# Kernel tuning notes

Hardware: AMD Instinct MI355X
Metric: run time of the kernel (lower is better)

Reference implementation:

```python
import jax, jax.numpy as jnp
import numpy as np

D_MODEL = 512
D_INNER = 1024           # expand=2 * d_model
HEADDIM = 1024           # headdim = 2*hidden_dim -> nheads = 1
NHEADS = 1
D_STATE = 128            # Mamba2 default
D_CONV = 4               # Mamba2 default
CONV_DIM = D_INNER + 2 * D_STATE   # 1280
D_IN_PROJ = 2 * D_INNER + 2 * D_STATE + NHEADS  # 2305
BATCH, SEQ = 8, 2048
EPS = 1e-5


def setup_inputs() -> dict:
    key = jax.random.key(0)
    ks = jax.random.split(key, 8)
    x = jax.random.normal(ks[0], (BATCH, SEQ, D_MODEL), dtype=jnp.float32)
    rnn_state = jnp.zeros((1, BATCH, D_MODEL), dtype=jnp.float32)
    W_in = jax.random.normal(ks[1], (D_MODEL, D_IN_PROJ), dtype=jnp.float32) * 0.02
    conv_w = jax.random.normal(ks[2], (CONV_DIM, D_CONV), dtype=jnp.float32) * 0.2
    conv_b = jnp.zeros((CONV_DIM,), dtype=jnp.float32)
    dt_bias = jax.random.normal(ks[3], (NHEADS,), dtype=jnp.float32) * 0.1
    # A in (-16, -1): A_log = log(uniform(1,16))
    A_log = jnp.log(jax.random.uniform(ks[4], (NHEADS,), minval=1.0, maxval=16.0, dtype=jnp.float32))
    D = jnp.ones((NHEADS,), dtype=jnp.float32)
    norm_w = jnp.ones((D_INNER,), dtype=jnp.float32)
    W_out = jax.random.normal(ks[5], (D_INNER, D_MODEL), dtype=jnp.float32) * 0.02
    return {"x": x, "rnn_state": rnn_state, "W_in": W_in, "conv_w": conv_w,
            "conv_b": conv_b, "dt_bias": dt_bias, "A_log": A_log, "D": D,
            "norm_w": norm_w, "W_out": W_out}


def _mamba2_forward(x, W_in, conv_w, conv_b, dt_bias, A_log, D, norm_w, W_out):
    Bsz, T, _ = x.shape
    zxbcdt = x @ W_in                              # [B,T,2305]
    z = zxbcdt[..., :D_INNER]                      # [B,T,1024]
    xBC = zxbcdt[..., D_INNER:D_INNER + CONV_DIM]  # [B,T,1280]
    dt = zxbcdt[..., -NHEADS:]                     # [B,T,1]

    # causal depthwise conv1d over time, then silu
    xBC_t = jnp.transpose(xBC, (0, 2, 1))          # [B,C,T]
    w = conv_w[:, None, :]                          # [C,1,K]
    conv = jax.lax.conv_general_dilated(
        xBC_t, w, window_strides=(1,), padding=[(D_CONV - 1, 0)],
        feature_group_count=CONV_DIM, dimension_numbers=("NCH", "OIH", "NCH"))
    xBC = jax.nn.silu(jnp.transpose(conv, (0, 2, 1)) + conv_b)  # [B,T,1280]

    x_ssm = xBC[..., :D_INNER].reshape(Bsz, T, NHEADS, HEADDIM)  # [B,T,H,P]
    Bm = xBC[..., D_INNER:D_INNER + D_STATE]       # [B,T,N] (ngroups=1)
    Cm = xBC[..., -D_STATE:]                       # [B,T,N]

    dt = jax.nn.softplus(dt + dt_bias)             # [B,T,H]
    A = -jnp.exp(A_log)                            # [H]

    # selective SSM recurrence over time (time-major scan)
    xs = (jnp.transpose(x_ssm, (1, 0, 2, 3)),      # [T,B,H,P]
          jnp.transpose(dt, (1, 0, 2)),            # [T,B,H]
          jnp.transpose(Bm, (1, 0, 2)),            # [T,B,N]
          jnp.transpose(Cm, (1, 0, 2)))            # [T,B,N]
    h0 = jnp.zeros((Bsz, NHEADS, HEADDIM, D_STATE), dtype=x.dtype)

    def step(h, inp):
        xt, dtt, Bt, Ct = inp
        dA = jnp.exp(dtt * A)                      # [B,H]
        h = h * dA[:, :, None, None] + (dtt[:, :, None] * xt)[..., None] * Bt[:, None, None, :]
        y = jnp.einsum("bhpn,bn->bhp", h, Ct)
        return h, y

    _, ys = jax.lax.scan(step, h0, xs)             # ys: [T,B,H,P]
    y = jnp.transpose(ys, (1, 0, 2, 3)) + x_ssm * D[None, None, :, None]
    y = y.reshape(Bsz, T, D_INNER)

    # gated RMSNorm (norm_before_gate=False): rmsnorm(y * silu(z)) * weight
    y = y * jax.nn.silu(z)
    y = y * jax.lax.rsqrt(jnp.mean(y * y, axis=-1, keepdims=True) + EPS) * norm_w
    return y @ W_out                               # [B,T,D_MODEL]


def reference(x, rnn_state, W_in, conv_w, conv_b, dt_bias, A_log, D, norm_w, W_out):
    out = _mamba2_forward(x, W_in, conv_w, conv_b, dt_bias, A_log, D, norm_w, W_out)
    return (out, rnn_state)
```

## Files before the change

kernel.cpp:

```cpp
#include <hip/hip_runtime.h>
#include <hip/hip_bf16.h>
#include <math.h>

#define D_MODEL 512
#define D_INNER 1024
#define D_STATE 128
#define CONV_DIM (D_INNER + 2*D_STATE)
#define D_IN_PROJ (2*D_INNER + 2*D_STATE + 1)
#define NPROJ 2304
#define BATCH 8
#define SEQ 2048
#define NROWS (BATCH*SEQ)
#define CHUNK 128
#define NCHUNK (NROWS/CHUNK)
#define CPB (SEQ/CHUNK)
#define EPS_RMS 1e-5f

typedef __hip_bfloat16 bf16;
typedef __attribute__((ext_vector_type(8))) short short8;
typedef __attribute__((ext_vector_type(4))) float f32x4;

__device__ __forceinline__ float fbf(bf16 v) { return __bfloat162float(v); }
__device__ __forceinline__ bf16 tbf(float v) { return __float2bfloat16(v); }
__device__ __forceinline__ float fexp(float x) { return __expf(x); }
__device__ __forceinline__ float frcp(float x) { return __builtin_amdgcn_rcpf(x); }
__device__ __forceinline__ float fsilu(float a) { return a * frcp(1.f + fexp(-a)); }

__device__ __forceinline__ void gl2lds16(const bf16* g, bf16* l) {
    __builtin_amdgcn_global_load_lds(
        (const __attribute__((address_space(1))) unsigned int*)g,
        (__attribute__((address_space(3))) unsigned int*)l, 16, 0, 0);
}

__global__ __launch_bounds__(256) void k_prologue(
    const float* __restrict__ W_in, const float* __restrict__ W_out,
    const float* __restrict__ norm_w, const float* __restrict__ rnn,
    bf16* __restrict__ W_inbT, bf16* __restrict__ W_outbT, float* __restrict__ outTail)
{
    int b = blockIdx.x;
    if (b == 1152 + 512) {
        int tid = threadIdx.x;
        #pragma unroll
        for (int i = 0; i < 4; ++i)
            *(float4*)(outTail + (tid + i * 256) * 4) =
                *(const float4*)(rnn + (tid + i * 256) * 4);
        return;
    }
    __shared__ float tile[32][33];
    const float* src; bf16* dst; const float* scale;
    int c0, r0, sstride, C;
    if (b < 1152) {
        src = W_in; dst = W_inbT; scale = nullptr;
        c0 = (b % 16) * 32; r0 = (b / 16) * 32; sstride = D_IN_PROJ; C = D_MODEL;
    } else {
        int bb = b - 1152;
        src = W_out; dst = W_outbT; scale = norm_w;
        c0 = (bb % 32) * 32; r0 = (bb / 32) * 32; sstride = D_MODEL; C = D_INNER;
    }
    int tx = threadIdx.x & 31, ty = threadIdx.x >> 5;
    #pragma unroll
    for (int i = 0; i < 32; i += 8) {
        float s = scale ? scale[c0 + ty + i] : 1.f;
        tile[ty + i][tx] = src[(size_t)(c0 + ty + i) * sstride + (r0 + tx)] * s;
    }
    __syncthreads();
    #pragma unroll
    for (int i = 0; i < 32; i += 8)
        dst[(size_t)(r0 + ty + i) * C + (c0 + tx)] = tbf(tile[tx][ty + i]);
}

__global__ __launch_bounds__(256) void k_dtcvt(
    const float* __restrict__ x, const float* __restrict__ W_in,
    const float* __restrict__ dt_bias,
    bf16* __restrict__ xb, float* __restrict__ dts, float* __restrict__ ssq)
{
    __shared__ float wcol[D_MODEL];
    int tid = threadIdx.x;
    wcol[tid]       = W_in[(size_t)tid * D_IN_PROJ + 2304];
    wcol[tid + 256] = W_in[(size_t)(tid + 256) * D_IN_PROJ + 2304];
    __syncthreads();
    int row  = blockIdx.x * 4 + (tid >> 6);
    int lane = tid & 63;
    const float* xr = x + (size_t)row * D_MODEL;
    float4 a = *(const float4*)(xr + lane * 8);
    float4 b = *(const float4*)(xr + lane * 8 + 4);
    union { bf16 o[8]; uint4 u; } pk;
    pk.o[0]=tbf(a.x); pk.o[1]=tbf(a.y); pk.o[2]=tbf(a.z); pk.o[3]=tbf(a.w);
    pk.o[4]=tbf(b.x); pk.o[5]=tbf(b.y); pk.o[6]=tbf(b.z); pk.o[7]=tbf(b.w);
    *(uint4*)(xb + (size_t)row * D_MODEL + lane * 8) = pk.u;
    const float* wc = wcol + lane * 8;
    float s = a.x*wc[0]+a.y*wc[1]+a.z*wc[2]+a.w*wc[3]
            + b.x*wc[4]+b.y*wc[5]+b.z*wc[6]+b.w*wc[7];
    #pragma unroll
    for (int off = 32; off; off >>= 1) s += __shfl_xor(s, off);
    if (lane == 0) {
        float raw = s + dt_bias[0];
        dts[row] = raw > 20.f ? raw : log1pf(fexp(raw));
        ssq[row] = 0.f;
    }
}

template<int MODE>
__global__ __launch_bounds__(256) void k_bgemm(
    const bf16* __restrict__ A, int lda, size_t sA,
    const bf16* __restrict__ Bt, int ldb, size_t sB,
    void* __restrict__ Cv, int ldc, size_t sC, int K,
    const bf16* __restrict__ zg, float* __restrict__ ssq)
{
    constexpr int BK = 64;
    __shared__ __align__(16) bf16 SM[128 * 128];
    bf16* As = SM;
    bf16* Bs = SM + 8192;
    const int tid = threadIdx.x, lane = tid & 63, wave = tid >> 6;
    const int wm = (wave & 1) * 64, wn = (wave >> 1) * 64;
    const int lr = lane & 15, quad = lane >> 4;
    const int rx = lr & 7;
    const size_t bm = (size_t)blockIdx.x * 128;
    const size_t bn = (size_t)blockIdx.y * 128;
    const size_t bi = blockIdx.z;
    A  += bi * sA;
    Bt += bi * sB;
    const int srow = lane >> 3;
    const int scol = (((lane & 7) ^ srow) << 3);

    f32x4 acc[4][4];
    #pragma unroll
    for (int i = 0; i < 4; ++i)
        #pragma unroll
        for (int j = 0; j < 4; ++j) acc[i][j] = (f32x4){0.f,0.f,0.f,0.f};

    for (int k0 = 0; k0 < K; k0 += BK) {
        __syncthreads();
        #pragma unroll
        for (int q = 0; q < 4; ++q) {
            int rg = wave * 32 + q * 8;
            gl2lds16(A  + (bm + rg + srow) * lda + k0 + scol, As + rg * BK);
            gl2lds16(Bt + (bn + rg + srow) * ldb + k0 + scol, Bs + rg * BK);
        }
        __syncthreads();
        #pragma unroll
        for (int ks = 0; ks < BK; ks += 32) {
            const int off = ((((ks >> 3) + quad) ^ rx) << 3);
            short8 af[4], bg[4];
            #pragma unroll
            for (int i = 0; i < 4; ++i)
                af[i] = *(const short8*)(As + (wm + i*16 + lr) * BK + off);
            #pragma unroll
            for (int j = 0; j < 4; ++j)
                bg[j] = *(const short8*)(Bs + (wn + j*16 + lr) * BK + off);
            #pragma unroll
            for (int i = 0; i < 4; ++i)
                #pragma unroll
                for (int j = 0; j < 4; ++j)
                    acc[i][j] = __builtin_amdgcn_mfma_f32_16x16x32_bf16(af[i], bg[j], acc[i][j], 0,0,0);
        }
    }
    if (MODE <= 1) {
        #pragma unroll
        for (int i = 0; i < 4; ++i)
            #pragma unroll
            for (int j = 0; j < 4; ++j)
                #pragma unroll
                for (int r = 0; r < 4; ++r) {
                    size_t row = bm + wm + i*16 + quad*4 + r;
                    size_t col = bn + wn + j*16 + lr;
                    float v = acc[i][j][r];
                    if (MODE == 0) ((float*)Cv + bi*sC)[row * ldc + col] = v;
                    else           ((bf16*)Cv + bi*sC)[row * ldc + col] = tbf(v);
                }
    } else if (MODE == 2) {
        const size_t tokbase = bi * CHUNK;
        const bf16* zrow = zg + tokbase * D_INNER + bn;
        __syncthreads();
        #pragma unroll
        for (int q = 0; q < 8; ++q) {
            int r0 = wave * 32 + q * 4;
            int rr = r0 + (lane >> 4);
            int gl = (lane & 15) ^ (rr & 7);
            gl2lds16(zrow + (size_t)rr * D_INNER + gl * 8, SM + r0 * 128);
        }
        __syncthreads();
        float srw[4][4];
        #pragma unroll
        for (int i = 0; i < 4; ++i)
            #pragma unroll
            for (int r = 0; r < 4; ++r) srw[i][r] = 0.f;
        #pragma unroll
        for (int i = 0; i < 4; ++i)
            #pragma unroll
            for (int j = 0; j < 4; ++j)
                #pragma unroll
                for (int r = 0; r < 4; ++r) {
                    int row = wm + i*16 + quad*4 + r;
                    int col = wn + j*16 + lr;
                    int gph = ((col >> 3) ^ (row & 7));
                    float z = fbf(SM[row * 128 + (gph << 3) + (col & 7)]);
                    float g = acc[i][j][r] * z * frcp(1.f + fexp(-z));
                    ((bf16*)Cv + bi*sC)[(size_t)row * ldc + bn + col] = tbf(g);
                    srw[i][r] += g * g;
                }
        #pragma unroll
        for (int i = 0; i < 4; ++i)
            #pragma unroll
            for (int r = 0; r < 4; ++r) {
                float s = srw[i][r];
                s += __shfl_xor(s, 1);
                s += __shfl_xor(s, 2);
                s += __shfl_xor(s, 4);
                s += __shfl_xor(s, 8);
                if (lr == 0)
                    atomicAdd(ssq + tokbase + wm + i*16 + quad*4 + r, s);
            }
    } else {
        #pragma unroll
        for (int i = 0; i < 4; ++i)
            #pragma unroll
            for (int r = 0; r < 4; ++r) {
                size_t row = bm + wm + i*16 + quad*4 + r;
                float sc = rsqrtf(ssq[row] * (1.f / D_INNER) + EPS_RMS);
                #pragma unroll
                for (int j = 0; j < 4; ++j) {
                    size_t col = bn + wn + j*16 + lr;
                    ((float*)Cv + bi*sC)[row * ldc + col] = acc[i][j][r] * sc;
                }
            }
    }
}

__global__ __launch_bounds__(256) void k_gemm_in(
    const bf16* __restrict__ A, const bf16* __restrict__ Bt,
    bf16* __restrict__ zb, bf16* __restrict__ xBCin, int K)
{
    constexpr int BK = 64;
    __shared__ __align__(16) bf16 As[128][BK];
    __shared__ __align__(16) bf16 Bs[128][BK];
    const int tid = threadIdx.x, lane = tid & 63, wave = tid >> 6;
    const int wm = (wave & 1) * 64, wn = (wave >> 1) * 64;
    const int lr = lane & 15, quad = lane >> 4;
    const int rx = lr & 7;
    const size_t bm = (size_t)blockIdx.x * 128;
    const int bn = blockIdx.y * 128;
    const int srow = lane >> 3;
    const int scol = (((lane & 7) ^ srow) << 3);

    f32x4 acc[4][4];
    #pragma unroll
    for (int i = 0; i < 4; ++i)
        #pragma unroll
        for (int j = 0; j < 4; ++j) acc[i][j] = (f32x4){0.f,0.f,0.f,0.f};

    for (int k0 = 0; k0 < K; k0 += BK) {
        __syncthreads();
        #pragma unroll
        for (int q = 0; q < 4; ++q) {
            int rg = wave * 32 + q * 8;
            gl2lds16(A  + (bm + rg + srow) * K + k0 + scol, &As[rg][0]);
            gl2lds16(Bt + ((size_t)bn + rg + srow) * K + k0 + scol, &Bs[rg][0]);
        }
        __syncthreads();
        #pragma unroll
        for (int ks = 0; ks < BK; ks += 32) {
            const int off = ((((ks >> 3) + quad) ^ rx) << 3);
            short8 af[4], bg[4];
            #pragma unroll
            for (int i = 0; i < 4; ++i)
                af[i] = *(const short8*)(&As[wm + i*16 + lr][off]);
            #pragma unroll
            for (int j = 0; j < 4; ++j)
                bg[j] = *(const short8*)(&Bs[wn + j*16 + lr][off]);
            #pragma unroll
            for (int i = 0; i < 4; ++i)
                #pragma unroll
                for (int j = 0; j < 4; ++j)
                    acc[i][j] = __builtin_amdgcn_mfma_f32_16x16x32_bf16(af[i], bg[j], acc[i][j], 0,0,0);
        }
    }
    #pragma unroll
    for (int i = 0; i < 4; ++i)
        #pragma unroll
        for (int j = 0; j < 4; ++j)
            #pragma unroll
            for (int r = 0; r < 4; ++r) {
                size_t row = bm + wm + i*16 + quad*4 + r;
                int col = bn + wn + j*16 + lr;
                float v = acc[i][j][r];
                if (col < D_INNER) zb[row * D_INNER + col] = tbf(v);
                else xBCin[row * CONV_DIM + (col - D_INNER)] = tbf(v);
            }
}

__global__ void k_prep(const float* __restrict__ dts, const float* __restrict__ A_log,
                       float* __restrict__ svec, float* __restrict__ wvec,
                       float* __restrict__ esvec, float* __restrict__ Pc)
{
    int chunk = blockIdx.x, t = threadIdx.x;
    int row = chunk * CHUNK + t;
    float A = -fexp(A_log[0]);
    __shared__ float sh[CHUNK];
    sh[t] = A * dts[row];
    __syncthreads();
    for (int off = 1; off < CHUNK; off <<= 1) {
        float v = (t >= off) ? sh[t - off] : 0.f;
        __syncthreads();
        sh[t] += v;
        __syncthreads();
    }
    float s = sh[t], sL = sh[CHUNK - 1];
    svec[row]  = s;
    wvec[row]  = fexp(sL - s) * dts[row];
    esvec[row] = fexp(s);
    if (t == CHUNK - 1) Pc[chunk] = fexp(sL);
}

__global__ __launch_bounds__(256) void k_ssd_bc(
    const bf16* __restrict__ xBCin, const float* __restrict__ conv_w,
    const float* __restrict__ conv_b, const float* __restrict__ wvec,
    const float* __restrict__ esvec, const float* __restrict__ svec,
    const float* __restrict__ dts, const float* __restrict__ Dp,
    bf16* __restrict__ Bw, bf16* __restrict__ A2)
{
    __shared__ __align__(16) bf16 Ls[131][128];
    __shared__ __align__(16) bf16 Bts[128][136];
    __shared__ __align__(16) bf16 Cts[128][136];
    __shared__ float sv_s[128], dt_s[128], wv_s[128], es_s[128];
    const int chunk = blockIdx.x;
    const int tid = threadIdx.x;
    const bool first = (chunk % CPB) == 0;
    const size_t rowbase = (size_t)chunk * CHUNK;
    if (tid < 128) {
        sv_s[tid] = svec[rowbase + tid];
        dt_s[tid] = dts[rowbase + tid];
        wv_s[tid] = wvec[rowbase + tid];
        es_s[tid] = esvec[rowbase + tid];
    }
    const int ch  = tid & 127;
    const int seg = tid >> 7;

    #pragma unroll
    for (int phase = 0; phase < 2; ++phase) {
        const int coff = D_INNER + phase * 128;
        __syncthreads();
        for (int i = tid; i < 131 * 16; i += 256) {
            int r = i >> 4, cg = (i & 15) << 3;
            uint4 v = (uint4){0,0,0,0};
            if (!(first && r < 3))
                v = *(const uint4*)(xBCin + (rowbase + r - 3) * CONV_DIM + coff + cg);
            *(uint4*)(&Ls[r][cg]) = v;
        }
        __syncthreads();
        float4 w = *(const float4*)(conv_w + (coff + ch) * 4);
        float bias = conv_b[coff + ch];
        float xv[11];
        #pragma unroll
        for (int i = 0; i < 3; ++i) xv[i + 8] = fbf(Ls[seg * 64 + i][ch]);
        for (int v = 0; v < 8; ++v) {
            int t0 = seg * 64 + v * 8;
            xv[0]=xv[8]; xv[1]=xv[9]; xv[2]=xv[10];
            #pragma unroll
            for (int i = 3; i < 11; ++i) xv[i] = fbf(Ls[t0 + i][ch]);
            float o[8];
            #pragma unroll
            for (int j = 0; j < 8; ++j) {
                float a = bias + w.x*xv[j] + w.y*xv[j+1] + w.z*xv[j+2] + w.w*xv[j+3];
                o[j] = fsilu(a);
            }
            if (phase == 0) {
                union { bf16 ob[8]; uint4 u; } pk;
                #pragma unroll
                for (int j = 0; j < 8; ++j) {
                    Bts[t0 + j][ch] = tbf(o[j]);
                    pk.ob[j] = tbf(o[j] * wv_s[t0 + j]);
                }
                *(uint4*)(Bw + (size_t)chunk*(D_STATE*CHUNK) + (size_t)ch*CHUNK + t0) = pk.u;
            } else {
                #pragma unroll
                for (int j = 0; j < 8; ++j) {
                    Cts[t0 + j][ch] = tbf(o[j]);
                    A2[(size_t)chunk*(CHUNK*256) + (size_t)(t0+j)*256 + 128 + ch] =
                        tbf(o[j] * es_s[t0 + j]);
                }
            }
        }
    }
    __syncthreads();
    const int lane = tid & 63, wave = tid >> 6;
    const int wm = (wave & 1) * 64, wn = (wave >> 1) * 64;
    const int lr = lane & 15, quad = lane >> 4;
    f32x4 acc[4][4];
    #pragma unroll
    for (int i = 0; i < 4; ++i)
        #pragma unroll
        for (int j = 0; j < 4; ++j) acc[i][j] = (f32x4){0.f,0.f,0.f,0.f};
    #pragma unroll
    for (int ks = 0; ks < 128; ks += 32) {
        short8 af[4], bg[4];
        #pragma unroll
        for (int i = 0; i < 4; ++i)
            af[i] = *(const short8*)(&Cts[wm + i*16 + lr][ks + quad*8]);
        #pragma unroll
        for (int j = 0; j < 4; ++j)
            bg[j] = *(const short8*)(&Bts[wn + j*16 + lr][ks + quad*8]);
        #pragma unroll
        for (int i = 0; i < 4; ++i)
            #pragma unroll
            for (int j = 0; j < 4; ++j)
                acc[i][j] = __builtin_amdgcn_mfma_f32_16x16x32_bf16(af[i], bg[j], acc[i][j], 0,0,0);
    }
    const float D0 = Dp[0];
    #pragma unroll
    for (int i = 0; i < 4; ++i)
        #pragma unroll
        for (int j = 0; j < 4; ++j)
            #pragma unroll
            for (int r = 0; r < 4; ++r) {
                int t = wm + i*16 + quad*4 + r;
                int u = wn + j*16 + lr;
                float o = 0.f;
                if (u <= t) {
                    o = acc[i][j][r] * fexp(sv_s[t] - sv_s[u]) * dt_s[u];
                    if (u == t) o += D0;
                }
                A2[(size_t)chunk*(CHUNK*256) + (size_t)t*256 + u] = tbf(o);
            }
}

__global__ __launch_bounds__(256) void k_conv_xdh(
    const bf16* __restrict__ xBCin, const float* __restrict__ conv_w,
    const float* __restrict__ conv_b, const bf16* __restrict__ Bw,
    bf16* __restrict__ B2, bf16* __restrict__ dH)
{
    __shared__ __align__(16) bf16 Ls[131][128];
    __shared__ __align__(16) bf16 XsF[128 * 128];
    const int chunk = blockIdx.y;
    const int p0 = blockIdx.x * 128;
    const int tid = threadIdx.x;
    const bool first = (chunk % CPB) == 0;
    const size_t rowbase = (size_t)chunk * CHUNK;
    for (int i = tid; i < 131 * 16; i += 256) {
        int r = i >> 4, cg = (i & 15) << 3;
        uint4 v = (uint4){0,0,0,0};
        if (!(first && r < 3))
            v = *(const uint4*)(xBCin + (rowbase + r - 3) * CONV_DIM + p0 + cg);
        *(uint4*)(&Ls[r][cg]) = v;
    }
    __syncthreads();
    const int p = tid & 127;
    const int half = tid >> 7;
    const int ch = p0 + p;
    float4 w = *(const float4*)(conv_w + ch * 4);
    float bias = conv_b[ch];
    bf16* outrow = B2 + (size_t)chunk * (D_INNER * 256) + (size_t)ch * 256;
    float xv[11];
    #pragma unroll
    for (int i = 0; i < 3; ++i) xv[i + 8] = fbf(Ls[half * 64 + i][p]);
    for (int v = 0; v < 8; ++v) {
        int t0 = half * 64 + v * 8;
        xv[0]=xv[8]; xv[1]=xv[9]; xv[2]=xv[10];
        #pragma unroll
        for (int i = 3; i < 11; ++i) xv[i] = fbf(Ls[t0 + i][p]);
        union { bf16 o[8]; uint4 u; } pk;
        #pragma unroll
        for (int j = 0; j < 8; ++j) {
            float a = bias + w.x*xv[j] + w.y*xv[j+1] + w.z*xv[j+2] + w.w*xv[j+3];
            pk.o[j] = tbf(fsilu(a));
        }
        *(uint4*)(outrow + t0) = pk.u;
        *(uint4*)(&XsF[p * 128 + ((((t0 >> 3) ^ (p & 7))) << 3)]) = pk.u;
    }
    __syncthreads();
    const int lane = tid & 63, wave = tid >> 6;
    const int wm = (wave & 1) * 64, wn = (wave >> 1) * 64;
    const int lr = lane & 15, quad = lane >> 4;
    const bf16* bwc = Bw + (size_t)chunk * (D_STATE * CHUNK);
    f32x4 acc[4][4];
    #pragma unroll
    for (int i = 0; i < 4; ++i)
        #pragma unroll
        for (int j = 0; j < 4; ++j) acc[i][j] = (f32x4){0.f,0.f,0.f,0.f};
    #pragma unroll
    for (int ks = 0; ks < 128; ks += 32) {
        short8 af[4], bg[4];
        #pragma unroll
        for (int j = 0; j < 4; ++j)
            bg[j] = *(const short8*)(bwc + (size_t)(wn + j*16 + lr) * CHUNK + ks + quad*8);
        #pragma unroll
        for (int i = 0; i < 4; ++i)
            af[i] = *(const short8*)(&XsF[(wm + i*16 + lr) * 128 +
                                          (((((ks >> 3) + quad) ^ (lr & 7))) << 3)]);
        #pragma unroll
        for (int i = 0; i < 4; ++i)
            #pragma unroll
            for (int j = 0; j < 4; ++j)
                acc[i][j] = __builtin_amdgcn_mfma_f32_16x16x32_bf16(af[i], bg[j], acc[i][j], 0,0,0);
    }
    #pragma unroll
    for (int i = 0; i < 4; ++i)
        #pragma unroll
        for (int j = 0; j < 4; ++j)
            #pragma unroll
            for (int r = 0; r < 4; ++r) {
                int pr = p0 + wm + i*16 + quad*4 + r;
                int n  = wn + j*16 + lr;
                dH[(size_t)chunk*(D_INNER*D_STATE) + (size_t)pr*D_STATE + n] = tbf(acc[i][j][r]);
            }
}

__global__ __launch_bounds__(256) void k_carry(
    const bf16* __restrict__ dH, const float* __restrict__ Pc, bf16* __restrict__ B2)
{
    int idx = blockIdx.x * 256 + threadIdx.x;
    int b = blockIdx.y;
    int p = idx >> 4, ng = (idx & 15) << 3;
    uint4 v[CPB];
    float pc[CPB];
    #pragma unroll
    for (int c = 0; c < CPB; ++c)
        v[c] = *(const uint4*)(dH + (size_t)(b*CPB + c)*(D_INNER*D_STATE) + (size_t)p*D_STATE + ng);
    #pragma unroll
    for (int c = 0; c < CPB; ++c) pc[c] = Pc[b*CPB + c];
    float h[8] = {0,0,0,0,0,0,0,0};
    #pragma unroll
    for (int c = 0; c < CPB; ++c) {
        union { bf16 o[8]; uint4 u; } pk;
        #pragma unroll
        for (int k = 0; k < 8; ++k) pk.o[k] = tbf(h[k]);
        *(uint4*)(B2 + (size_t)(b*CPB + c)*(D_INNER*256) + (size_t)p*256 + 128 + ng) = pk.u;
        const bf16* vb = (const bf16*)&v[c];
        #pragma unroll
        for (int k = 0; k < 8; ++k) h[k] = pc[c]*h[k] + fbf(vb[k]);
    }
}

extern "C" void kernel_launch(void* const* d_in, const int* in_sizes, int n_in,
                              void* d_out, int out_size, void* d_ws, size_t ws_size,
                              hipStream_t stream)
{
    const float* x       = (const float*)d_in[0];
    const float* rnn     = (const float*)d_in[1];
    const float* W_in    = (const float*)d_in[2];
    const float* conv_w  = (const float*)d_in[3];
    const float* conv_b  = (const float*)d_in[4];
    const float* dt_bias = (const float*)d_in[5];
    const float* A_log   = (const float*)d_in[6];
    const float* Dp      = (const float*)d_in[7];
    const float* norm_w  = (const float*)d_in[8];
    const float* W_out   = (const float*)d_in[9];
    float* out = (float*)d_out;

    char* ws = (char*)d_ws;
    size_t off = 0;
    auto alloc = [&](size_t bytes) { void* p = ws + off; off += (bytes + 255) & ~255ULL; return p; };

    bf16*  W_inbT  = (bf16*) alloc((size_t)NPROJ * D_MODEL * 2);
    bf16*  W_outbT = (bf16*) alloc((size_t)D_MODEL * D_INNER * 2);
    float* dts     = (float*)alloc((size_t)NROWS * 4);
    float* svec    = (float*)alloc((size_t)NROWS * 4);
    float* wvec    = (float*)alloc((size_t)NROWS * 4);
    float* esvec   = (float*)alloc((size_t)NROWS * 4);
    float* Pc      = (float*)alloc((size_t)NCHUNK * 4);
    float* ssq     = (float*)alloc((size_t)NROWS * 4);
    bf16*  zb      = (bf16*) alloc((size_t)NROWS * D_INNER * 2);
    bf16*  A2      = (bf16*) alloc((size_t)NCHUNK * CHUNK * 256 * 2);
    bf16*  B2      = (bf16*) alloc((size_t)NCHUNK * D_INNER * 256 * 2);
    bf16*  Bw      = (bf16*) alloc((size_t)NCHUNK * D_STATE * CHUNK * 2);
    char* RA = (char*)alloc((size_t)NROWS * D_MODEL * 2 + (size_t)NROWS * D_INNER * 2);
    bf16*  xb   = (bf16*)RA;
    bf16*  dH   = (bf16*)(RA + (size_t)NROWS * D_MODEL * 2);
    bf16*  ybf  = (bf16*)RA;
    bf16*  xBCin = (bf16*)alloc((size_t)NROWS * CONV_DIM * 2);

    k_dtcvt<<<NROWS / 4, 256, 0, stream>>>(x, W_in, dt_bias, xb, dts, ssq);
    k_prologue<<<1152 + 512 + 1, 256, 0, stream>>>(
        W_in, W_out, norm_w, rnn, W_inbT, W_outbT, out + (size_t)NROWS * D_MODEL);
    k_prep<<<NCHUNK, CHUNK, 0, stream>>>(dts, A_log, svec, wvec, esvec, Pc);

    k_gemm_in<<<dim3(NROWS/128, NPROJ/128), 256, 0, stream>>>(xb, W_inbT, zb, xBCin, D_MODEL);

    k_ssd_bc<<<NCHUNK, 256, 0, stream>>>(xBCin, conv_w, conv_b, wvec, esvec,
                                         svec, dts, Dp, Bw, A2);

    k_conv_xdh<<<dim3(8, NCHUNK), 256, 0, stream>>>(xBCin, conv_w, conv_b, Bw, B2, dH);

    k_carry<<<dim3(64, BATCH), 256, 0, stream>>>(dH, Pc, B2);

    k_bgemm<2><<<dim3(1, D_INNER/128, NCHUNK), 256, 0, stream>>>(
        A2, 256, (size_t)CHUNK*256,
        B2, 256, (size_t)D_INNER*256,
        ybf, D_INNER, (size_t)CHUNK*D_INNER, 256, zb, ssq);

    k_bgemm<3><<<dim3(NROWS/128, D_MODEL/128, 1), 256, 0, stream>>>(
        ybf, D_INNER, 0, W_outbT, D_INNER, 0, out, D_MODEL, 0, D_INNER,
        nullptr, ssq);
}
```

Baseline: 297.0 us.

## Rewrite input-projection GEMM with 256x256 tiles and double-buffered LDS prefetch

Enlarges the in-projection GEMM block tile from 128x128 to 256x256 with 512 threads and 8x4 accumulator fragments per wave. The K loop now double-buffers shared memory and interleaves the global-to-LDS prefetch of the next tile with four MFMA phases, using explicit waitcnt, sched barriers and setprio. The aim is to hide global load latency and raise data reuse. In exchange it uses 128KB of LDS and many more registers, which lowers occupancy, and grid parallelism drops to 64x9 blocks.

```diff
diff --git a/kernel.cpp b/kernel.cpp
--- a/kernel.cpp
+++ b/kernel.cpp
@@ -227,66 +227,158 @@
     }
 }
 
-__global__ __launch_bounds__(256) void k_gemm_in(
+__global__ __launch_bounds__(512, 2) void k_gemm_in(
     const bf16* __restrict__ A, const bf16* __restrict__ Bt,
-    bf16* __restrict__ zb, bf16* __restrict__ xBCin, int K)
+    bf16* __restrict__ zb, bf16* __restrict__ xBCin)
 {
     constexpr int BK = 64;
-    __shared__ __align__(16) bf16 As[128][BK];
-    __shared__ __align__(16) bf16 Bs[128][BK];
+    constexpr int NT = D_MODEL / BK;
+    __shared__ __align__(16) bf16 SM[4 * 256 * BK];
+    bf16* const As0 = SM;
+    bf16* const Bs0 = SM + 16384;
+    bf16* const As1 = SM + 32768;
+    bf16* const Bs1 = SM + 49152;
+
     const int tid = threadIdx.x, lane = tid & 63, wave = tid >> 6;
-    const int wm = (wave & 1) * 64, wn = (wave >> 1) * 64;
+    const int wm = (wave >> 2) * 128;
+    const int wn = (wave & 3) * 64;
     const int lr = lane & 15, quad = lane >> 4;
     const int rx = lr & 7;
-    const size_t bm = (size_t)blockIdx.x * 128;
-    const int bn = blockIdx.y * 128;
+    const size_t bm = (size_t)blockIdx.x * 256;
+    const int    bn = blockIdx.y * 256;
     const int srow = lane >> 3;
-    const int scol = (((lane & 7) ^ srow) << 3);
-
-    f32x4 acc[4][4];
-    #pragma unroll
-    for (int i = 0; i < 4; ++i)
+    const int scol = ((lane & 7) ^ srow) << 3;
+
+    f32x4 acc[8][4];
+    #pragma unroll
+    for (int i = 0; i < 8; ++i)
         #pragma unroll
         for (int j = 0; j < 4; ++j) acc[i][j] = (f32x4){0.f,0.f,0.f,0.f};
 
-    for (int k0 = 0; k0 < K; k0 += BK) {
-        __syncthreads();
-        #pragma unroll
-        for (int q = 0; q < 4; ++q) {
-            int rg = wave * 32 + q * 8;
-            gl2lds16(A  + (bm + rg + srow) * K + k0 + scol, &As[rg][0]);
-            gl2lds16(Bt + ((size_t)bn + rg + srow) * K + k0 + scol, &Bs[rg][0]);
+    auto stage = [&](bf16* Ad, bf16* Bd, int k0, int p) {
+        const int rg = (wave << 5) + (p << 3);
+        gl2lds16(A  + (bm + rg + srow) * D_MODEL + k0 + scol, Ad + rg * BK);
+        gl2lds16(Bt + (size_t)(bn + rg + srow) * D_MODEL + k0 + scol, Bd + rg * BK);
+    };
+    auto rdA = [&](const bf16* base, int i, int s) {
+        return *(const short8*)(base + (wm + i*16 + lr) * BK + ((((s << 2) + quad) ^ rx) << 3));
+    };
+    auto rdB = [&](const bf16* base, int j, int s) {
+        return *(const short8*)(base + (wn + j*16 + lr) * BK + ((((s << 2) + quad) ^ rx) << 3));
+    };
+
+    #pragma unroll
+    for (int p = 0; p < 4; ++p) stage(As0, Bs0, 0, p);
+
+    short8 af[4][2], bgA[2][2], bgB[2][2];
+
+    #pragma unroll 1
+    for (int kt = 0; kt < NT; ++kt) {
+        bf16* Ac = (kt & 1) ? As1 : As0;
+        bf16* Bc = (kt & 1) ? Bs1 : Bs0;
+        bf16* An = (kt & 1) ? As0 : As1;
+        bf16* Bn = (kt & 1) ? Bs0 : Bs1;
+        const int  kn = (kt + 1) * BK;
+        const bool pf = kt < NT - 1;
+
+        if (pf) {
+            stage(An, Bn, kn, 0);
+            asm volatile("s_waitcnt vmcnt(2)" ::: "memory");
+        } else {
+            asm volatile("s_waitcnt vmcnt(0)" ::: "memory");
         }
-        __syncthreads();
-        #pragma unroll
-        for (int ks = 0; ks < BK; ks += 32) {
-            const int off = ((((ks >> 3) + quad) ^ rx) << 3);
-            short8 af[4], bg[4];
-            #pragma unroll
-            for (int i = 0; i < 4; ++i)
-                af[i] = *(const short8*)(&As[wm + i*16 + lr][off]);
-            #pragma unroll
-            for (int j = 0; j < 4; ++j)
-                bg[j] = *(const short8*)(&Bs[wn + j*16 + lr][off]);
-            #pragma unroll
-            for (int i = 0; i < 4; ++i)
-                #pragma unroll
-                for (int j = 0; j < 4; ++j)
-                    acc[i][j] = __builtin_amdgcn_mfma_f32_16x16x32_bf16(af[i], bg[j], acc[i][j], 0,0,0);
-        }
-    }
-    #pragma unroll
-    for (int i = 0; i < 4; ++i)
-        #pragma unroll
-        for (int j = 0; j < 4; ++j)
+        __builtin_amdgcn_s_barrier();
+        __builtin_amdgcn_sched_barrier(0);
+        #pragma unroll
+        for (int i = 0; i < 4; ++i) { af[i][0] = rdA(Ac, i, 0); af[i][1] = rdA(Ac, i, 1); }
+        #pragma unroll
+        for (int j = 0; j < 2; ++j) { bgA[j][0] = rdB(Bc, j, 0); bgA[j][1] = rdB(Bc, j, 1); }
+        asm volatile("s_waitcnt lgkmcnt(0)" ::: "memory");
+        __builtin_amdgcn_sched_barrier(0);
+        __builtin_amdgcn_s_setprio(1);
+        #pragma unroll
+        for (int i = 0; i < 4; ++i)
+            #pragma unroll
+            for (int j = 0; j < 2; ++j) {
+                acc[i][j] = __builtin_amdgcn_mfma_f32_16x16x32_bf16(af[i][0], bgA[j][0], acc[i][j], 0,0,0);
+                acc[i][j] = __builtin_amdgcn_mfma_f32_16x16x32_bf16(af[i][1], bgA[j][1], acc[i][j], 0,0,0);
+            }
+        __builtin_amdgcn_s_setprio(0);
+        __builtin_amdgcn_s_barrier();
+
+        #pragma unroll
+        for (int j = 0; j < 2; ++j) { bgB[j][0] = rdB(Bc, 2 + j, 0); bgB[j][1] = rdB(Bc, 2 + j, 1); }
+        if (pf) stage(An, Bn, kn, 1);
+        __builtin_amdgcn_s_barrier();
+        asm volatile("s_waitcnt lgkmcnt(0)" ::: "memory");
+        __builtin_amdgcn_sched_barrier(0);
+        __builtin_amdgcn_s_setprio(1);
+        #pragma unroll
+        for (int i = 0; i < 4; ++i)
+            #pragma unroll
+            for (int j = 0; j < 2; ++j) {
+                acc[i][2+j] = __builtin_amdgcn_mfma_f32_16x16x32_bf16(af[i][0], bgB[j][0], acc[i][2+j], 0,0,0);
+                acc[i][2+j] = __builtin_amdgcn_mfma_f32_16x16x32_bf16(af[i][1], bgB[j][1], acc[i][2+j], 0,0,0);
+            }
+        __builtin_amdgcn_s_setprio(0);
+        __builtin_amdgcn_s_barrier();
+
+        #pragma unroll
+        for (int i = 0; i < 4; ++i) { af[i][0] = rdA(Ac, 4 + i, 0); af[i][1] = rdA(Ac, 4 + i, 1); }
+        if (pf) stage(An, Bn, kn, 2);
+        __builtin_amdgcn_s_barrier();
+        asm volatile("s_waitcnt lgkmcnt(0)" ::: "memory");
+        __builtin_amdgcn_sched_barrier(0);
+        __builtin_amdgcn_s_setprio(1);
+        #pragma unroll
+        for (int i = 0; i < 4; ++i)
+            #pragma unroll
+            for (int j = 0; j < 2; ++j) {
+                acc[4+i][j] = __builtin_amdgcn_mfma_f32_16x16x32_bf16(af[i][0], bgA[j][0], acc[4+i][j], 0,0,0);
+                acc[4+i][j] = __builtin_amdgcn_mfma_f32_16x16x32_bf16(af[i][1], bgA[j][1], acc[4+i][j], 0,0,0);
+            }
+        __builtin_amdgcn_s_setprio(0);
+        __builtin_amdgcn_s_barrier();
+
+        if (pf) stage(An, Bn, kn, 3);
+        __builtin_amdgcn_s_barrier();
+        __builtin_amdgcn_sched_barrier(0);
+        __builtin_amdgcn_s_setprio(1);
+        #pragma unroll
+        for (int i = 0; i < 4; ++i)
+            #pragma unroll
+            for (int j = 0; j < 2; ++j) {
+                acc[4+i][2+j] = __builtin_amdgcn_mfma_f32_16x16x32_bf16(af[i][0], bgB[j][0], acc[4+i][2+j], 0,0,0);
+                acc[4+i][2+j] = __builtin_amdgcn_mfma_f32_16x16x32_bf16(af[i][1], bgB[j][1], acc[4+i][2+j], 0,0,0);
+            }
+        __builtin_amdgcn_s_setprio(0);
+        __builtin_amdgcn_s_barrier();
+    }
+
+    if (bn < D_INNER) {
+        #pragma unroll
+        for (int i = 0; i < 8; ++i)
             #pragma unroll
             for (int r = 0; r < 4; ++r) {
                 size_t row = bm + wm + i*16 + quad*4 + r;
-                int col = bn + wn + j*16 + lr;
-                float v = acc[i][j][r];
-                if (col < D_INNER) zb[row * D_INNER + col] = tbf(v);
-                else xBCin[row * CONV_DIM + (col - D_INNER)] = tbf(v);
-            }
+                bf16* orow = zb + row * D_INNER + bn + wn;
+                #pragma unroll
+                for (int j = 0; j < 4; ++j)
+                    orow[j*16 + lr] = tbf(acc[i][j][r]);
+            }
+    } else {
+        const int cb = bn - D_INNER;
+        #pragma unroll
+        for (int i = 0; i < 8; ++i)
+            #pragma unroll
+            for (int r = 0; r < 4; ++r) {
+                size_t row = bm + wm + i*16 + quad*4 + r;
+                bf16* orow = xBCin + row * CONV_DIM + cb + wn;
+                #pragma unroll
+                for (int j = 0; j < 4; ++j)
+                    orow[j*16 + lr] = tbf(acc[i][j][r]);
+            }
+    }
 }
 
 __global__ void k_prep(const float* __restrict__ dts, const float* __restrict__ A_log,
@@ -574,7 +666,7 @@
         W_in, W_out, norm_w, rnn, W_inbT, W_outbT, out + (size_t)NROWS * D_MODEL);
     k_prep<<<NCHUNK, CHUNK, 0, stream>>>(dts, A_log, svec, wvec, esvec, Pc);
 
-    k_gemm_in<<<dim3(NROWS/128, NPROJ/128), 256, 0, stream>>>(xb, W_inbT, zb, xBCin, D_MODEL);
+    k_gemm_in<<<dim3(NROWS/256, NPROJ/256), 512, 0, stream>>>(xb, W_inbT, zb, xBCin);
 
     k_ssd_bc<<<NCHUNK, 256, 0, stream>>>(xBCin, conv_w, conv_b, wvec, esvec,
                                          svec, dts, Dp, Bw, A2);
```

Measured after the change: 296.8 us. No clear change (-0.1%).

## Double-buffer LDS tiles with async prefetch in bf16 GEMM kernels

Applied to the files above, without the earlier changes.

Both MFMA GEMM kernels now keep two LDS tile buffers and issue global-to-LDS loads two K-steps ahead. Partial vmcnt waits plus raw s_barrier replace the full __syncthreads pairs, so the loads for the next tile overlap with the MFMA work on the current one. The input-projection GEMM also makes K a compile-time constant. The cost is double the LDS per block (64KB), which may lower occupancy, and hand-written waitcnt counts that have to match the number of loads in flight.

```diff
diff --git a/kernel.cpp b/kernel.cpp
--- a/kernel.cpp
+++ b/kernel.cpp
@@ -108,9 +108,7 @@
     const bf16* __restrict__ zg, float* __restrict__ ssq)
 {
     constexpr int BK = 64;
-    __shared__ __align__(16) bf16 SM[128 * 128];
-    bf16* As = SM;
-    bf16* Bs = SM + 8192;
+    __shared__ __align__(16) bf16 SM[4 * 8192];
     const int tid = threadIdx.x, lane = tid & 63, wave = tid >> 6;
     const int wm = (wave & 1) * 64, wn = (wave >> 1) * 64;
     const int lr = lane & 15, quad = lane >> 4;
@@ -129,15 +127,26 @@
         #pragma unroll
         for (int j = 0; j < 4; ++j) acc[i][j] = (f32x4){0.f,0.f,0.f,0.f};
 
-    for (int k0 = 0; k0 < K; k0 += BK) {
-        __syncthreads();
+    auto stage = [&](bf16* Ad, bf16* Bd, int k0) {
         #pragma unroll
         for (int q = 0; q < 4; ++q) {
             int rg = wave * 32 + q * 8;
-            gl2lds16(A  + (bm + rg + srow) * lda + k0 + scol, As + rg * BK);
-            gl2lds16(Bt + (bn + rg + srow) * ldb + k0 + scol, Bs + rg * BK);
-        }
-        __syncthreads();
+            gl2lds16(A  + (bm + rg + srow) * lda + k0 + scol, Ad + rg * BK);
+            gl2lds16(Bt + (bn + rg + srow) * ldb + k0 + scol, Bd + rg * BK);
+        }
+    };
+
+    const int NT = K / BK;
+    stage(SM, SM + 8192, 0);
+    if (NT > 1) stage(SM + 16384, SM + 24576, BK);
+
+    for (int kt = 0; kt < NT; ++kt) {
+        if (kt + 1 < NT) asm volatile("s_waitcnt vmcnt(8)" ::: "memory");
+        else             asm volatile("s_waitcnt vmcnt(0)" ::: "memory");
+        __builtin_amdgcn_s_barrier();
+        __builtin_amdgcn_sched_barrier(0);
+        const bf16* As = SM + (kt & 1) * 16384;
+        const bf16* Bs = As + 8192;
         #pragma unroll
         for (int ks = 0; ks < BK; ks += 32) {
             const int off = ((((ks >> 3) + quad) ^ rx) << 3);
@@ -153,6 +162,12 @@
                 #pragma unroll
                 for (int j = 0; j < 4; ++j)
                     acc[i][j] = __builtin_amdgcn_mfma_f32_16x16x32_bf16(af[i], bg[j], acc[i][j], 0,0,0);
+        }
+        __builtin_amdgcn_sched_barrier(0);
+        __builtin_amdgcn_s_barrier();
+        if (kt + 2 < NT) {
+            bf16* An = SM + (kt & 1) * 16384;
+            stage(An, An + 8192, (kt + 2) * BK);
         }
     }
     if (MODE <= 1) {
@@ -229,11 +244,12 @@
 
 __global__ __launch_bounds__(256) void k_gemm_in(
     const bf16* __restrict__ A, const bf16* __restrict__ Bt,
-    bf16* __restrict__ zb, bf16* __restrict__ xBCin, int K)
+    bf16* __restrict__ zb, bf16* __restrict__ xBCin)
 {
     constexpr int BK = 64;
-    __shared__ __align__(16) bf16 As[128][BK];
-    __shared__ __align__(16) bf16 Bs[128][BK];
+    constexpr int K = D_MODEL;
+    constexpr int NT = K / BK;
+    __shared__ __align__(16) bf16 SM[4 * 8192];
     const int tid = threadIdx.x, lane = tid & 63, wave = tid >> 6;
     const int wm = (wave & 1) * 64, wn = (wave >> 1) * 64;
     const int lr = lane & 15, quad = lane >> 4;
@@ -249,30 +265,46 @@
         #pragma unroll
         for (int j = 0; j < 4; ++j) acc[i][j] = (f32x4){0.f,0.f,0.f,0.f};
 
-    for (int k0 = 0; k0 < K; k0 += BK) {
-        __syncthreads();
+    auto stage = [&](bf16* Ad, bf16* Bd, int k0) {
         #pragma unroll
         for (int q = 0; q < 4; ++q) {
             int rg = wave * 32 + q * 8;
-            gl2lds16(A  + (bm + rg + srow) * K + k0 + scol, &As[rg][0]);
-            gl2lds16(Bt + ((size_t)bn + rg + srow) * K + k0 + scol, &Bs[rg][0]);
-        }
-        __syncthreads();
+            gl2lds16(A  + (bm + rg + srow) * K + k0 + scol, Ad + rg * BK);
+            gl2lds16(Bt + ((size_t)bn + rg + srow) * K + k0 + scol, Bd + rg * BK);
+        }
+    };
+
+    stage(SM, SM + 8192, 0);
+    stage(SM + 16384, SM + 24576, BK);
+
+    for (int kt = 0; kt < NT; ++kt) {
+        if (kt + 1 < NT) asm volatile("s_waitcnt vmcnt(8)" ::: "memory");
+        else             asm volatile("s_waitcnt vmcnt(0)" ::: "memory");
+        __builtin_amdgcn_s_barrier();
+        __builtin_amdgcn_sched_barrier(0);
+        const bf16* As = SM + (kt & 1) * 16384;
+        const bf16* Bs = As + 8192;
         #pragma unroll
         for (int ks = 0; ks < BK; ks += 32) {
             const int off = ((((ks >> 3) + quad) ^ rx) << 3);
             short8 af[4], bg[4];
             #pragma unroll
             for (int i = 0; i < 4; ++i)
-                af[i] = *(const short8*)(&As[wm + i*16 + lr][off]);
+                af[i] = *(const short8*)(As + (wm + i*16 + lr) * BK + off);
             #pragma unroll
             for (int j = 0; j < 4; ++j)
-                bg[j] = *(const short8*)(&Bs[wn + j*16 + lr][off]);
+                bg[j] = *(const short8*)(Bs + (wn + j*16 + lr) * BK + off);
             #pragma unroll
             for (int i = 0; i < 4; ++i)
                 #pragma unroll
                 for (int j = 0; j < 4; ++j)
                     acc[i][j] = __builtin_amdgcn_mfma_f32_16x16x32_bf16(af[i], bg[j], acc[i][j], 0,0,0);
+        }
+        __builtin_amdgcn_sched_barrier(0);
+        __builtin_amdgcn_s_barrier();
+        if (kt + 2 < NT) {
+            bf16* An = SM + (kt & 1) * 16384;
+            stage(An, An + 8192, (kt + 2) * BK);
         }
     }
     #pragma unroll
@@ -574,7 +606,7 @@
         W_in, W_out, norm_w, rnn, W_inbT, W_outbT, out + (size_t)NROWS * D_MODEL);
     k_prep<<<NCHUNK, CHUNK, 0, stream>>>(dts, A_log, svec, wvec, esvec, Pc);
 
-    k_gemm_in<<<dim3(NROWS/128, NPROJ/128), 256, 0, stream>>>(xb, W_inbT, zb, xBCin, D_MODEL);
+    k_gemm_in<<<dim3(NROWS/128, NPROJ/128), 256, 0, stream>>>(xb, W_inbT, zb, xBCin);
 
     k_ssd_bc<<<NCHUNK, 256, 0, stream>>>(xBCin, conv_w, conv_b, wvec, esvec,
                                          svec, dts, Dp, Bw, A2);
```

New measurement: 282.1 us. 5.0% less time.
